# Kernel tuning notes

Hardware: AMD Instinct MI355X
Metric: run time of the kernel (lower is better)

Reference implementation:

```python
import jax, jax.numpy as jnp
import numpy as np

D_MODEL = 256
D_STATE = 64
D_CONV = 4
EXPAND = 2
HEADDIM = 64
D_INNER = EXPAND * D_MODEL          # 512
NHEADS = D_INNER // HEADDIM         # 8
CONV_CH = D_INNER + 2 * D_STATE     # 640 (x, B, C channels go through depthwise conv)
D_IN_PROJ = 2 * D_INNER + 2 * D_STATE + NHEADS  # 1160


def _dwconv_causal(x, w, b):
    # x: (b, L, ch); w: (ch, 1, k) depthwise; left-pad k-1 -> causal, same as torch pad+truncate
    out = jax.lax.conv_general_dilated(
        x.transpose(0, 2, 1), w, (1,), [(D_CONV - 1, 0)],
        dimension_numbers=('NCH', 'OIH', 'NCH'), feature_group_count=CONV_CH)
    return out.transpose(0, 2, 1) + b


def _mamba2(u, in_w, conv_w, conv_b, dt_bias, A_log, D, norm_w, out_w):
    # u: (b, L, d_model). Faithful Mamba2 block (ngroups=1, rmsnorm gated, no proj biases).
    b, L, _ = u.shape
    zxbcdt = u @ in_w.T                                   # (b, L, 1160)
    z = zxbcdt[..., :D_INNER]
    xBC = zxbcdt[..., D_INNER:D_INNER + CONV_CH]
    dt = zxbcdt[..., D_INNER + CONV_CH:]                  # (b, L, h)
    xBC = jax.nn.silu(_dwconv_causal(xBC, conv_w, conv_b))
    x = xBC[..., :D_INNER].reshape(b, L, NHEADS, HEADDIM)  # (b, L, h, p)
    Bm = xBC[..., D_INNER:D_INNER + D_STATE]              # (b, L, n)
    Cm = xBC[..., D_INNER + D_STATE:]                     # (b, L, n)
    dt = jax.nn.softplus(dt + dt_bias)                    # (b, L, h)
    dA = jnp.exp(dt * (-jnp.exp(A_log)))                  # (b, L, h)

    def step(h, inp):
        dA_t, x_t, B_t, dt_t, C_t = inp
        # h: (b, heads, p, n) selective-scan state
        h = h * dA_t[:, :, None, None] + (dt_t[:, :, None] * x_t)[..., None] * B_t[:, None, None, :]
        return h, jnp.einsum('bhpn,bn->bhp', h, C_t)

    h0 = jnp.zeros((b, NHEADS, HEADDIM, D_STATE), u.dtype)
    xs = (dA.transpose(1, 0, 2), x.transpose(1, 0, 2, 3), Bm.transpose(1, 0, 2),
          dt.transpose(1, 0, 2), Cm.transpose(1, 0, 2))
    _, ys = jax.lax.scan(step, h0, xs)                    # (L, b, h, p)
    y = ys.transpose(1, 0, 2, 3) + x * D[None, None, :, None]
    y = y.reshape(b, L, D_INNER) * jax.nn.silu(z)         # gated
    y = y * jax.lax.rsqrt(jnp.mean(y * y, axis=-1, keepdims=True) + 1e-5) * norm_w
    return y @ out_w.T                                    # (b, L, d_model)


def setup_inputs() -> dict:
    key = jax.random.key(0)
    ks = jax.random.split(key, 20)
    def mk(i, shape, s=0.02):
        return jax.random.normal(ks[i], shape, jnp.float32) * s
    inp = {"x": jax.random.normal(ks[0], (8, 64, 64, D_MODEL), jnp.float32)}
    for pre, off in (("mh", 1), ("mv", 9)):
        inp[pre + "_in_w"] = mk(off, (D_IN_PROJ, D_MODEL))
        inp[pre + "_conv_w"] = mk(off + 1, (CONV_CH, 1, D_CONV), 0.2)
        inp[pre + "_conv_b"] = jnp.zeros((CONV_CH,), jnp.float32)
        inp[pre + "_dt_bias"] = mk(off + 3, (NHEADS,), 0.5)
        inp[pre + "_A_log"] = jnp.log(jax.random.uniform(ks[off + 4], (NHEADS,), jnp.float32, 1.0, 16.0))
        inp[pre + "_D"] = jnp.ones((NHEADS,), jnp.float32)
        inp[pre + "_norm_w"] = jnp.ones((D_INNER,), jnp.float32)
        inp[pre + "_out_w"] = mk(off + 7, (D_MODEL, D_INNER))
    inp["fc_w"] = mk(17, (D_MODEL, 4 * D_MODEL))
    inp["fc_b"] = jnp.zeros((D_MODEL,), jnp.float32)
    return inp


def reference(x, mh_in_w, mh_conv_w, mh_conv_b, mh_dt_bias, mh_A_log, mh_D, mh_norm_w, mh_out_w,
              mv_in_w, mv_conv_w, mv_conv_b, mv_dt_bias, mv_A_log, mv_D, mv_norm_w, mv_out_w,
              fc_w, fc_b):
    B, H, W, C = x.shape
    mh = (mh_in_w, mh_conv_w, mh_conv_b, mh_dt_bias, mh_A_log, mh_D, mh_norm_w, mh_out_w)
    mv = (mv_in_w, mv_conv_w, mv_conv_b, mv_dt_bias, mv_A_log, mv_D, mv_norm_w, mv_out_w)
    # horizontal: rows as sequences
    x_h = x.reshape(B * H, W, C)
    h1 = _mamba2(x_h, *mh)
    # NOTE: source flips dims=[0] (merged batch*row axis), replicated faithfully
    h2 = jnp.flip(_mamba2(jnp.flip(x_h, axis=0), *mh), axis=0)
    h = jnp.concatenate([h1, h2], axis=-1).reshape(B, H, W, -1)
    # vertical: columns as sequences
    x_v = x.transpose(0, 2, 1, 3).reshape(B * W, H, C)
    v1 = _mamba2(x_v, *mv)
    v2 = jnp.flip(_mamba2(jnp.flip(x_v, axis=0), *mv), axis=0)
    v = jnp.concatenate([v1, v2], axis=-1).reshape(B, W, H, -1).transpose(0, 2, 1, 3)
    out = jnp.concatenate([v, h], axis=-1)                # (B, H, W, 4*d_model)
    return out @ fc_w.T + fc_b                            # (B, H, W, d_model)
```

## Files before the change

kernel.cpp:

```cpp
#include <hip/hip_runtime.h>
#include <hip/hip_bf16.h>


#define NTH 512

typedef __attribute__((ext_vector_type(8))) short short8;
typedef __attribute__((ext_vector_type(4))) short short4v;
typedef __attribute__((ext_vector_type(4))) float floatx4;

__device__ __forceinline__ short f2bs(float v){
  __hip_bfloat16 h = __float2bfloat16(v);
  return *reinterpret_cast<short*>(&h);
}
__device__ __forceinline__ unsigned int pk2(float lo, float hi){
  return (unsigned int)(unsigned short)f2bs(lo)
       | ((unsigned int)(unsigned short)f2bs(hi) << 16);
}
__device__ __forceinline__ float bs2f(short s){
  union { unsigned int u; float f; } c; c.u = ((unsigned int)(unsigned short)s) << 16; return c.f;
}
__device__ __forceinline__ float bhi(unsigned int u){
  union { unsigned int u; float f; } c; c.u = u & 0xffff0000u; return c.f;
}
__device__ __forceinline__ float blo(unsigned int u){
  union { unsigned int u; float f; } c; c.u = u << 16; return c.f;
}
__device__ __forceinline__ float silu_f(float v){
  return v * __builtin_amdgcn_rcpf(1.f + __expf(-v));
}
__device__ __forceinline__ float softplus_f(float v){
  return fmaxf(v, 0.f) + log1pf(__expf(-fabsf(v)));
}

__global__ void setup_weights(const float* __restrict__ fc_w,
                              const float* __restrict__ how, const float* __restrict__ hnw,
                              const float* __restrict__ vow, const float* __restrict__ vnw,
                              const float* __restrict__ hw, const float* __restrict__ vw,
                              __hip_bfloat16* __restrict__ Wc,
                              __hip_bfloat16* __restrict__ inw)
{
  int b = blockIdx.x;
  if (b < 512) {
    __shared__ float fs[2][256];
    int dir = b >> 8;
    int rr = b & 255;
    int o0 = (rr >> 1) * 2;
    int j = (rr & 1) * 256 + threadIdx.x;
    const float* ow = dir ? vow : how;
    const float* nw = dir ? vnw : hnw;
    int off = dir ? 0 : 512;
    const float* fr0 = fc_w + o0 * 1024 + off;
    const float* fr1 = fc_w + (o0 + 1) * 1024 + off;
    fs[0][threadIdx.x] = fr0[threadIdx.x] + fr0[256 + threadIdx.x];
    fs[1][threadIdx.x] = fr1[threadIdx.x] + fr1[256 + threadIdx.x];
    __syncthreads();
    float a00 = 0.f, a01 = 0.f, a02 = 0.f, a03 = 0.f;
    float a10 = 0.f, a11 = 0.f, a12 = 0.f, a13 = 0.f;
#pragma unroll 4
    for (int k = 0; k < 256; k += 4) {
      float w0 = ow[(k + 0) * 512 + j];
      float w1 = ow[(k + 1) * 512 + j];
      float w2 = ow[(k + 2) * 512 + j];
      float w3 = ow[(k + 3) * 512 + j];
      a00 += fs[0][k + 0] * w0; a01 += fs[0][k + 1] * w1;
      a02 += fs[0][k + 2] * w2; a03 += fs[0][k + 3] * w3;
      a10 += fs[1][k + 0] * w0; a11 += fs[1][k + 1] * w1;
      a12 += fs[1][k + 2] * w2; a13 += fs[1][k + 3] * w3;
    }
    float nwj = nw[j];
    Wc[(dir * 256 + o0) * 512 + j]     = __float2bfloat16(nwj * (a00 + a01 + a02 + a03));
    Wc[(dir * 256 + o0 + 1) * 512 + j] = __float2bfloat16(nwj * (a10 + a11 + a12 + a13));
  } else {
    int id = (b - 512) * 256 + threadIdx.x;
    int dir = id / 299008;
    int r = id % 299008;
    int row = r >> 8;
    const float* src = dir ? vw : hw;
    float v = (row < 1160) ? src[r] : 0.f;
    inw[id] = __float2bfloat16(v);
  }
}

#define OFS_U    0
#define OFS_R1   16896
#define OFS_BX0  25872
#define OFS_BX1  30480
#define OFS_CUM  35088
#define OFS_DT   36112
#define SM_SHORTS 36624

template<int DIR>
__global__ __launch_bounds__(NTH, 4)
void mamba_dir_kernel(const float* __restrict__ x,
                      const __hip_bfloat16* __restrict__ inw_bf,
                      const float* __restrict__ conv_w,
                      const float* __restrict__ conv_b,
                      const float* __restrict__ dt_bias,
                      const float* __restrict__ A_log,
                      const float* __restrict__ Dvec,
                      const __hip_bfloat16* __restrict__ Wc,
                      const float* __restrict__ fc_b,
                      float* __restrict__ out)
{
  __shared__ short sm[SM_SHORTS];
  short* smU  = sm + OFS_U;
  short* smR1 = sm + OFS_R1;
  short* smB  = sm + OFS_BX0;
  short* smM  = smB;
  short* smg  = smB;
  short* smC  = sm + OFS_BX1;
  short* smX  = smC;
  float* smCUM = (float*)(sm + OFS_CUM);
  short* smDT  = sm + OFS_DT;
  float* smF   = (float*)sm;

  const int tid = threadIdx.x;
  const int t = tid & 63;
  const int w = tid >> 6;
  const int lane15 = tid & 15;
  const int quad = (tid & 63) >> 4;
  const int s = blockIdx.x;

  auto MF = [](short8 a, short8 b, floatx4 c) -> floatx4 {
    return __builtin_amdgcn_mfma_f32_16x16x32_bf16(a, b, c, 0, 0, 0);
  };
  auto ldA_u = [&](int mt_, int kt) -> short8 {
    return *(const short8*)(smU + (mt_ * 16 + lane15) * 264 + kt * 32 + quad * 8);
  };
  auto ldB_w = [&](int row0, int kt) -> short8 {
    return *(const short8*)((const short*)inw_bf + (row0 + lane15) * 256 + kt * 32 + quad * 8);
  };
  auto ldB_wc = [&](int o0, int hd, int kt) -> short8 {
    return *(const short8*)((const short*)Wc + (o0 + lane15) * 512 + hd * 64 + kt * 32 + quad * 8);
  };
  auto ld72 = [&](const short* base, int row, int kt) -> short8 {
    return *(const short8*)(base + row * 72 + kt * 32 + quad * 8);
  };
  auto proj_tile = [&](int row0, short* dst, bool wr) {
    floatx4 a0 = (floatx4)0.f, a1 = (floatx4)0.f, a2 = (floatx4)0.f, a3 = (floatx4)0.f;
#pragma unroll
    for (int kt = 0; kt < 8; ++kt) {
      short8 b = ldB_w(row0, kt);
      a0 = MF(ldA_u(0, kt), b, a0);
      a1 = MF(ldA_u(1, kt), b, a1);
      a2 = MF(ldA_u(2, kt), b, a2);
      a3 = MF(ldA_u(3, kt), b, a3);
    }
    if (wr) {
      *(unsigned int*)(dst + 0)  = pk2(a0[0], a0[1]);
      *(unsigned int*)(dst + 2)  = pk2(a0[2], a0[3]);
      *(unsigned int*)(dst + 16) = pk2(a1[0], a1[1]);
      *(unsigned int*)(dst + 18) = pk2(a1[2], a1[3]);
      *(unsigned int*)(dst + 32) = pk2(a2[0], a2[1]);
      *(unsigned int*)(dst + 34) = pk2(a2[2], a2[3]);
      *(unsigned int*)(dst + 48) = pk2(a3[0], a3[1]);
      *(unsigned int*)(dst + 50) = pk2(a3[2], a3[3]);
    }
  };

  long ubase; int ustride;
  if (DIR == 0) { ubase = (long)s * 16384; ustride = 256; }
  else { ubase = (long)(s >> 6) * 1048576 + (long)(s & 63) * 256; ustride = 16384; }

  for (int i = tid; i < 4096; i += NTH) {
    int tt = i >> 6, c4 = (i & 63) * 4;
    const float4 xa = *(const float4*)(x + ubase + (long)tt * ustride + c4);
    uint2 pk; pk.x = pk2(xa.x, xa.y); pk.y = pk2(xa.z, xa.w);
    *(uint2*)((unsigned int*)smU + tt * 132 + (i & 63) * 2) = pk;
  }
  if (tid < 64) smF[tid * 132 + 128] = 0.f;
  __syncthreads();

  for (int jt = w; jt < 9; jt += 8) {
    int q = jt * 16 + lane15;
    proj_tile(1024 + jt * 16, smR1 + q * 66 + quad * 4, q < 136);
  }
  __syncthreads();

  {
    int q = tid & 127;
    int tg = tid >> 7;
    const float4 cw = *(const float4*)(conv_w + (512 + q) * 4);
    float cb = conv_b[512 + q];
    const short* rowp = smR1 + q * 66;
    short* dstB = (q < 64) ? (smB + q) : (smC + (q - 64));
#pragma unroll
    for (int k = 0; k < 4; ++k) {
      int t0 = tg * 4 + k;
      const short* bp = rowp + 4 * t0 - 4;
      unsigned int u0 = *(const unsigned int*)(bp + 0);
      unsigned int u1 = *(const unsigned int*)(bp + 2);
      unsigned int u2 = *(const unsigned int*)(bp + 4);
      unsigned int u3 = *(const unsigned int*)(bp + 6);
      float f1 = bhi(u0), f2 = blo(u1), f3 = bhi(u1), f4 = blo(u2);
      float f5 = bhi(u2), f6 = blo(u3), f7 = bhi(u3);
      if (t0 == 0) { f1 = 0.f; f2 = 0.f; f3 = 0.f; }
      float v0 = fmaf(cw.x, f1, fmaf(cw.y, f2, fmaf(cw.z, f3, fmaf(cw.w, f4, cb))));
      float v1 = fmaf(cw.x, f2, fmaf(cw.y, f3, fmaf(cw.z, f4, fmaf(cw.w, f5, cb))));
      float v2 = fmaf(cw.x, f3, fmaf(cw.y, f4, fmaf(cw.z, f5, fmaf(cw.w, f6, cb))));
      float v3 = fmaf(cw.x, f4, fmaf(cw.y, f5, fmaf(cw.z, f6, fmaf(cw.w, f7, cb))));
      int tt = 4 * t0;
      dstB[(tt + 0) * 72] = f2bs(silu_f(v0));
      dstB[(tt + 1) * 72] = f2bs(silu_f(v1));
      dstB[(tt + 2) * 72] = f2bs(silu_f(v2));
      dstB[(tt + 3) * 72] = f2bs(silu_f(v3));
    }
    float dtv = softplus_f(bs2f(smR1[(128 + w) * 66 + t]) + dt_bias[w]);
    smDT[w * 64 + t] = f2bs(dtv);
    float cum = -__expf(A_log[w]) * dtv;
#pragma unroll
    for (int off = 1; off < 64; off <<= 1) {
      float y = __shfl_up(cum, off, 64);
      if (t >= off) cum += y;
    }
    smCUM[w * 64 + t] = cum;
  }
  __syncthreads();

  const int mt = w >> 1, nt0 = (w & 1) * 2;
  floatx4 g0 = (floatx4)0.f, g1 = (floatx4)0.f;
#pragma unroll
  for (int kt = 0; kt < 2; ++kt) {
    short8 a  = ld72(smC, mt * 16 + lane15, kt);
    short8 b0 = ld72(smB, nt0 * 16 + lane15, kt);
    short8 b1 = ld72(smB, (nt0 + 1) * 16 + lane15, kt);
    g0 = MF(a, b0, g0); g1 = MF(a, b1, g1);
  }

  float ssqAcc = 0.f;
  floatx4 accO[4][2];
#pragma unroll
  for (int m = 0; m < 4; ++m) { accO[m][0] = (floatx4)0.f; accO[m][1] = (floatx4)0.f; }

  for (int hd = 0; hd < 8; ++hd) {
    {
      int row0 = (w < 4) ? (hd * 64 + w * 16) : (512 + hd * 64 + (w - 4) * 16);
      int q = ((w < 4) ? w * 16 : 64 + (w - 4) * 16) + lane15;
      proj_tile(row0, smR1 + q * 66 + quad * 4, true);
    }
    __syncthreads();

    {
      int p = t;
      int ch = hd * 64 + p;
      const float4 cw = *(const float4*)(conv_w + ch * 4);
      float cb = conv_b[ch];
      const short* rowp = smR1 + (64 + p) * 66;
      short* dstX = smX + p * 72;
#pragma unroll
      for (int k = 0; k < 2; ++k) {
        int t0 = w * 2 + k;
        const short* bp = rowp + 4 * t0 - 4;
        unsigned int u0 = *(const unsigned int*)(bp + 0);
        unsigned int u1 = *(const unsigned int*)(bp + 2);
        unsigned int u2 = *(const unsigned int*)(bp + 4);
        unsigned int u3 = *(const unsigned int*)(bp + 6);
        float f1 = bhi(u0), f2 = blo(u1), f3 = bhi(u1), f4 = blo(u2);
        float f5 = bhi(u2), f6 = blo(u3), f7 = bhi(u3);
        if (t0 == 0) { f1 = 0.f; f2 = 0.f; f3 = 0.f; }
        float v0 = fmaf(cw.x, f1, fmaf(cw.y, f2, fmaf(cw.z, f3, fmaf(cw.w, f4, cb))));
        float v1 = fmaf(cw.x, f2, fmaf(cw.y, f3, fmaf(cw.z, f4, fmaf(cw.w, f5, cb))));
        float v2 = fmaf(cw.x, f3, fmaf(cw.y, f4, fmaf(cw.z, f5, fmaf(cw.w, f6, cb))));
        float v3 = fmaf(cw.x, f4, fmaf(cw.y, f5, fmaf(cw.z, f6, fmaf(cw.w, f7, cb))));
        *(unsigned int*)(dstX + 4 * t0)     = pk2(silu_f(v0), silu_f(v1));
        *(unsigned int*)(dstX + 4 * t0 + 2) = pk2(silu_f(v2), silu_f(v3));
      }
      const float* cumh = smCUM + hd * 64;
      const short* dth  = smDT + hd * 64;
#pragma unroll
      for (int j = 0; j < 2; ++j) {
        floatx4 gv = j ? g1 : g0;
        int ss = (nt0 + j) * 16 + lane15;
        float cums = cumh[ss];
        float dts  = bs2f(dth[ss]);
#pragma unroll
        for (int r = 0; r < 4; ++r) {
          int tt = mt * 16 + quad * 4 + r;
          float m = (tt >= ss) ? __expf(cumh[tt] - cums) * dts * gv[r] : 0.f;
          smM[tt * 72 + ss] = f2bs(m);
        }
      }
    }
    __syncthreads();

    floatx4 y0 = (floatx4)0.f, y1 = (floatx4)0.f;
#pragma unroll
    for (int kt = 0; kt < 2; ++kt) {
      short8 a  = ld72(smM, mt * 16 + lane15, kt);
      short8 b0 = ld72(smX, nt0 * 16 + lane15, kt);
      short8 b1 = ld72(smX, (nt0 + 1) * 16 + lane15, kt);
      y0 = MF(a, b0, y0); y1 = MF(a, b1, y1);
    }
    __syncthreads();

    {
      float Dh = Dvec[hd];
#pragma unroll
      for (int j = 0; j < 2; ++j) {
        floatx4 yy = j ? y1 : y0;
        int p = (nt0 + j) * 16 + lane15;
        short4v xv4 = *(const short4v*)(smX + p * 72 + mt * 16 + quad * 4);
#pragma unroll
        for (int r = 0; r < 4; ++r) {
          int tr = mt * 16 + quad * 4 + r;
          float xv = bs2f(xv4[r]);
          float zv = bs2f(smR1[p * 66 + tr]);
          float g = (yy[r] + Dh * xv) * silu_f(zv);
          smg[tr * 72 + p] = f2bs(g);
        }
      }
    }
    __syncthreads();

    {
      short8 gv = *(const short8*)(smg + t * 72 + w * 8);
#pragma unroll
      for (int j = 0; j < 8; ++j) { float g = bs2f(gv[j]); ssqAcc += g * g; }
    }
#pragma unroll
    for (int kt = 0; kt < 2; ++kt) {
      short8 b0 = ldB_wc(w * 16, hd, kt);
      short8 b1 = ldB_wc((w + 8) * 16, hd, kt);
#pragma unroll
      for (int m = 0; m < 4; ++m) {
        short8 a = ld72(smg, m * 16 + lane15, kt);
        accO[m][0] = MF(a, b0, accO[m][0]);
        accO[m][1] = MF(a, b1, accO[m][1]);
      }
    }
  }

  atomicAdd(&smF[t * 132 + 128], ssqAcc);
  __syncthreads();
  if (tid < 64)
    smF[tid * 132 + 129] = rsqrtf(smF[tid * 132 + 128] * (1.f / 512.f) + 1e-5f);
  __syncthreads();

#pragma unroll
  for (int m = 0; m < 4; ++m) {
#pragma unroll
    for (int n = 0; n < 2; ++n) {
      int o = (w + n * 8) * 16 + lane15;
#pragma unroll
      for (int r = 0; r < 4; ++r) {
        int tt = m * 16 + quad * 4 + r;
        float val = accO[m][n][r] * smF[tt * 132 + 129];
        long rowg = (DIR == 0) ? ((long)s * 64 + tt)
                               : ((long)(s >> 6) * 4096 + (long)tt * 64 + (s & 63));
        long gi = rowg * 256 + o;
        if (DIR == 0) out[gi] = fc_b[o] + val;
        else          out[gi] += val;
      }
    }
  }
}

extern "C" void kernel_launch(void* const* d_in, const int* in_sizes, int n_in,
                              void* d_out, int out_size, void* d_ws, size_t ws_size,
                              hipStream_t stream) {
  const float* x          = (const float*)d_in[0];
  const float* mh_in_w    = (const float*)d_in[1];
  const float* mh_conv_w  = (const float*)d_in[2];
  const float* mh_conv_b  = (const float*)d_in[3];
  const float* mh_dt_bias = (const float*)d_in[4];
  const float* mh_A_log   = (const float*)d_in[5];
  const float* mh_D       = (const float*)d_in[6];
  const float* mh_norm_w  = (const float*)d_in[7];
  const float* mh_out_w   = (const float*)d_in[8];
  const float* mv_in_w    = (const float*)d_in[9];
  const float* mv_conv_w  = (const float*)d_in[10];
  const float* mv_conv_b  = (const float*)d_in[11];
  const float* mv_dt_bias = (const float*)d_in[12];
  const float* mv_A_log   = (const float*)d_in[13];
  const float* mv_D       = (const float*)d_in[14];
  const float* mv_norm_w  = (const float*)d_in[15];
  const float* mv_out_w   = (const float*)d_in[16];
  const float* fc_w       = (const float*)d_in[17];
  const float* fc_b       = (const float*)d_in[18];
  float* out = (float*)d_out;

  __hip_bfloat16* Wcb  = (__hip_bfloat16*)d_ws;
  __hip_bfloat16* inwb = (__hip_bfloat16*)((char*)d_ws + 524288);

  setup_weights<<<2848, 256, 0, stream>>>(fc_w, mh_out_w, mh_norm_w, mv_out_w, mv_norm_w,
                                          mh_in_w, mv_in_w, Wcb, inwb);
  mamba_dir_kernel<0><<<512, NTH, 0, stream>>>(x, inwb, mh_conv_w, mh_conv_b,
      mh_dt_bias, mh_A_log, mh_D, Wcb, fc_b, out);
  mamba_dir_kernel<1><<<512, NTH, 0, stream>>>(x, inwb + 299008, mv_conv_w, mv_conv_b,
      mv_dt_bias, mv_A_log, mv_D, Wcb + 131072, fc_b, out);
}
```

Before: 291.0 us.

## Fuse both scan directions into one launch with atomic output and 32x32 MFMA projections

Merges the horizontal and vertical Mamba kernels into a single 1024-block launch so both directions run concurrently instead of serially. The output is now pre-filled with fc_b in the setup kernel and both directions accumulate into it with float atomics. The in-projection tiles switch from 16x16x32 to 32x32x16 MFMA, which means fewer instructions and more reuse of the B operand. The cost is atomic traffic on the output and nondeterministic summation order.

```diff
diff --git a/kernel.cpp b/kernel.cpp
--- a/kernel.cpp
+++ b/kernel.cpp
@@ -7,6 +7,7 @@
 typedef __attribute__((ext_vector_type(8))) short short8;
 typedef __attribute__((ext_vector_type(4))) short short4v;
 typedef __attribute__((ext_vector_type(4))) float floatx4;
+typedef __attribute__((ext_vector_type(16))) float floatx16;
 
 __device__ __forceinline__ short f2bs(float v){
   __hip_bfloat16 h = __float2bfloat16(v);
@@ -36,8 +37,10 @@
                               const float* __restrict__ how, const float* __restrict__ hnw,
                               const float* __restrict__ vow, const float* __restrict__ vnw,
                               const float* __restrict__ hw, const float* __restrict__ vw,
+                              const float* __restrict__ fc_b,
                               __hip_bfloat16* __restrict__ Wc,
-                              __hip_bfloat16* __restrict__ inw)
+                              __hip_bfloat16* __restrict__ inw,
+                              float* __restrict__ out)
 {
   int b = blockIdx.x;
   if (b < 512) {
@@ -70,7 +73,7 @@
     float nwj = nw[j];
     Wc[(dir * 256 + o0) * 512 + j]     = __float2bfloat16(nwj * (a00 + a01 + a02 + a03));
     Wc[(dir * 256 + o0 + 1) * 512 + j] = __float2bfloat16(nwj * (a10 + a11 + a12 + a13));
-  } else {
+  } else if (b < 2848) {
     int id = (b - 512) * 256 + threadIdx.x;
     int dir = id / 299008;
     int r = id % 299008;
@@ -78,6 +81,10 @@
     const float* src = dir ? vw : hw;
     float v = (row < 1160) ? src[r] : 0.f;
     inw[id] = __float2bfloat16(v);
+  } else {
+    int id = (b - 2848) * 256 + threadIdx.x;
+    int i4 = id * 4;
+    *(float4*)(out + i4) = *(const float4*)(fc_b + (i4 & 255));
   }
 }
 
@@ -89,18 +96,16 @@
 #define OFS_DT   36112
 #define SM_SHORTS 36624
 
-template<int DIR>
 __global__ __launch_bounds__(NTH, 4)
-void mamba_dir_kernel(const float* __restrict__ x,
-                      const __hip_bfloat16* __restrict__ inw_bf,
-                      const float* __restrict__ conv_w,
-                      const float* __restrict__ conv_b,
-                      const float* __restrict__ dt_bias,
-                      const float* __restrict__ A_log,
-                      const float* __restrict__ Dvec,
-                      const __hip_bfloat16* __restrict__ Wc,
-                      const float* __restrict__ fc_b,
-                      float* __restrict__ out)
+void mamba_fused(const float* __restrict__ x,
+                 const __hip_bfloat16* __restrict__ inw_all,
+                 const float* __restrict__ hconv_w, const float* __restrict__ vconv_w,
+                 const float* __restrict__ hconv_b, const float* __restrict__ vconv_b,
+                 const float* __restrict__ hdt_b,  const float* __restrict__ vdt_b,
+                 const float* __restrict__ hA,     const float* __restrict__ vA,
+                 const float* __restrict__ hD,     const float* __restrict__ vD,
+                 const __hip_bfloat16* __restrict__ Wc_all,
+                 float* __restrict__ out)
 {
   __shared__ short sm[SM_SHORTS];
   short* smU  = sm + OFS_U;
@@ -119,16 +124,29 @@
   const int w = tid >> 6;
   const int lane15 = tid & 15;
   const int quad = (tid & 63) >> 4;
-  const int s = blockIdx.x;
+
+  const int DIR = blockIdx.x >> 9;
+  const int s = blockIdx.x & 511;
+
+  const __hip_bfloat16* inw = inw_all + DIR * 299008;
+  const __hip_bfloat16* Wc  = Wc_all  + DIR * 131072;
+  const float* conv_w  = DIR ? vconv_w : hconv_w;
+  const float* conv_b  = DIR ? vconv_b : hconv_b;
+  const float* dt_bias = DIR ? vdt_b  : hdt_b;
+  const float* A_log   = DIR ? vA     : hA;
+  const float* Dvec    = DIR ? vD     : hD;
 
   auto MF = [](short8 a, short8 b, floatx4 c) -> floatx4 {
     return __builtin_amdgcn_mfma_f32_16x16x32_bf16(a, b, c, 0, 0, 0);
   };
+  auto MF32 = [](short8 a, short8 b, floatx16 c) -> floatx16 {
+    return __builtin_amdgcn_mfma_f32_32x32x16_bf16(a, b, c, 0, 0, 0);
+  };
   auto ldA_u = [&](int mt_, int kt) -> short8 {
     return *(const short8*)(smU + (mt_ * 16 + lane15) * 264 + kt * 32 + quad * 8);
   };
   auto ldB_w = [&](int row0, int kt) -> short8 {
-    return *(const short8*)((const short*)inw_bf + (row0 + lane15) * 256 + kt * 32 + quad * 8);
+    return *(const short8*)((const short*)inw + (row0 + lane15) * 256 + kt * 32 + quad * 8);
   };
   auto ldB_wc = [&](int o0, int hd, int kt) -> short8 {
     return *(const short8*)((const short*)Wc + (o0 + lane15) * 512 + hd * 64 + kt * 32 + quad * 8);
@@ -158,6 +176,31 @@
     }
   };
 
+  const int ct  = w & 3;
+  const int mt2 = w >> 2;
+  const int lane31 = tid & 31;
+  const int half32 = (tid & 63) >> 5;
+  const short* A32 = smU + (mt2 * 32 + lane31) * 264 + half32 * 8;
+  auto proj32 = [&](int wrow0, int c0) {
+    const short* Bb = (const short*)inw + (wrow0 + lane31) * 256 + half32 * 8;
+    floatx16 aA = (floatx16)0.f, aB = (floatx16)0.f;
+#pragma unroll
+    for (int kt = 0; kt < 16; kt += 2) {
+      aA = MF32(*(const short8*)(A32 + kt * 16),      *(const short8*)(Bb + kt * 16),      aA);
+      aB = MF32(*(const short8*)(A32 + kt * 16 + 16), *(const short8*)(Bb + kt * 16 + 16), aB);
+    }
+    short* dst = smR1 + (c0 + lane31) * 66 + mt2 * 32 + 4 * half32;
+#pragma unroll
+    for (int g = 0; g < 4; ++g) {
+      float e0 = aA[4*g+0] + aB[4*g+0];
+      float e1 = aA[4*g+1] + aB[4*g+1];
+      float e2 = aA[4*g+2] + aB[4*g+2];
+      float e3 = aA[4*g+3] + aB[4*g+3];
+      *(unsigned int*)(dst + g * 8)     = pk2(e0, e1);
+      *(unsigned int*)(dst + g * 8 + 2) = pk2(e2, e3);
+    }
+  };
+
   long ubase; int ustride;
   if (DIR == 0) { ubase = (long)s * 16384; ustride = 256; }
   else { ubase = (long)(s >> 6) * 1048576 + (long)(s & 63) * 256; ustride = 16384; }
@@ -171,10 +214,9 @@
   if (tid < 64) smF[tid * 132 + 128] = 0.f;
   __syncthreads();
 
-  for (int jt = w; jt < 9; jt += 8) {
-    int q = jt * 16 + lane15;
-    proj_tile(1024 + jt * 16, smR1 + q * 66 + quad * 4, q < 136);
-  }
+  proj32(1024 + ct * 32, ct * 32);
+  if (w == 7)
+    proj_tile(1152, smR1 + (128 + lane15) * 66 + quad * 4, lane15 < 8);
   __syncthreads();
 
   {
@@ -234,9 +276,9 @@
 
   for (int hd = 0; hd < 8; ++hd) {
     {
-      int row0 = (w < 4) ? (hd * 64 + w * 16) : (512 + hd * 64 + (w - 4) * 16);
-      int q = ((w < 4) ? w * 16 : 64 + (w - 4) * 16) + lane15;
-      proj_tile(row0, smR1 + q * 66 + quad * 4, true);
+      int c0 = ct * 32;
+      int wrow0 = (c0 < 64) ? (hd * 64 + c0) : (512 + hd * 64 + (c0 - 64));
+      proj32(wrow0, c0);
     }
     __syncthreads();
 
@@ -347,9 +389,7 @@
         float val = accO[m][n][r] * smF[tt * 132 + 129];
         long rowg = (DIR == 0) ? ((long)s * 64 + tt)
                                : ((long)(s >> 6) * 4096 + (long)tt * 64 + (s & 63));
-        long gi = rowg * 256 + o;
-        if (DIR == 0) out[gi] = fc_b[o] + val;
-        else          out[gi] += val;
+        atomicAdd(&out[rowg * 256 + o], val);
       }
     }
   }
@@ -382,10 +422,10 @@
   __hip_bfloat16* Wcb  = (__hip_bfloat16*)d_ws;
   __hip_bfloat16* inwb = (__hip_bfloat16*)((char*)d_ws + 524288);
 
-  setup_weights<<<2848, 256, 0, stream>>>(fc_w, mh_out_w, mh_norm_w, mv_out_w, mv_norm_w,
-                                          mh_in_w, mv_in_w, Wcb, inwb);
-  mamba_dir_kernel<0><<<512, NTH, 0, stream>>>(x, inwb, mh_conv_w, mh_conv_b,
-      mh_dt_bias, mh_A_log, mh_D, Wcb, fc_b, out);
-  mamba_dir_kernel<1><<<512, NTH, 0, stream>>>(x, inwb + 299008, mv_conv_w, mv_conv_b,
-      mv_dt_bias, mv_A_log, mv_D, Wcb + 131072, fc_b, out);
-}
+  setup_weights<<<11040, 256, 0, stream>>>(fc_w, mh_out_w, mh_norm_w, mv_out_w, mv_norm_w,
+                                           mh_in_w, mv_in_w, fc_b, Wcb, inwb, out);
+  mamba_fused<<<1024, NTH, 0, stream>>>(x, inwb,
+      mh_conv_w, mv_conv_w, mh_conv_b, mv_conv_b,
+      mh_dt_bias, mv_dt_bias, mh_A_log, mv_A_log, mh_D, mv_D,
+      Wcb, out);
+}
```

Result: slower. 357.7 us (+22.9%).

## XOR-swizzle shared-memory tiles to avoid bank conflicts; vectorize weight conversion

Applied to the files above, without the earlier changes.

Applies an XOR swizzle to the LDS layouts of the input tile, the B/C/X buffers, the decay matrix and the gated output. Every writer and reader, including the MFMA operand loads, is updated to match. The goal is fewer bank conflicts on the 16-byte MFMA fragment loads and on the strided scalar stores. The weight-conversion part of setup_weights now handles 8 elements per thread with float4 loads and short8 stores, which shrinks that launch's grid. The risk is a correctness bug if any access to a swizzled buffer was missed, because all of them must agree.

```diff
diff --git a/kernel.cpp b/kernel.cpp
--- a/kernel.cpp
+++ b/kernel.cpp
@@ -71,13 +71,21 @@
     Wc[(dir * 256 + o0) * 512 + j]     = __float2bfloat16(nwj * (a00 + a01 + a02 + a03));
     Wc[(dir * 256 + o0 + 1) * 512 + j] = __float2bfloat16(nwj * (a10 + a11 + a12 + a13));
   } else {
-    int id = (b - 512) * 256 + threadIdx.x;
-    int dir = id / 299008;
-    int r = id % 299008;
+    int id8 = ((b - 512) * 256 + threadIdx.x) * 8;
+    int dir = id8 / 299008;
+    int r = id8 % 299008;
     int row = r >> 8;
     const float* src = dir ? vw : hw;
-    float v = (row < 1160) ? src[r] : 0.f;
-    inw[id] = __float2bfloat16(v);
+    short8 o;
+    if (row < 1160) {
+      const float4 x0 = *(const float4*)(src + r);
+      const float4 x1 = *(const float4*)(src + r + 4);
+      o[0] = f2bs(x0.x); o[1] = f2bs(x0.y); o[2] = f2bs(x0.z); o[3] = f2bs(x0.w);
+      o[4] = f2bs(x1.x); o[5] = f2bs(x1.y); o[6] = f2bs(x1.z); o[7] = f2bs(x1.w);
+    } else {
+      o = (short8)0;
+    }
+    *(short8*)((short*)inw + id8) = o;
   }
 }
 
@@ -125,7 +133,8 @@
     return __builtin_amdgcn_mfma_f32_16x16x32_bf16(a, b, c, 0, 0, 0);
   };
   auto ldA_u = [&](int mt_, int kt) -> short8 {
-    return *(const short8*)(smU + (mt_ * 16 + lane15) * 264 + kt * 32 + quad * 8);
+    return *(const short8*)(smU + (mt_ * 16 + lane15) * 264 + kt * 32
+                            + ((quad ^ (lane15 & 3)) << 3));
   };
   auto ldB_w = [&](int row0, int kt) -> short8 {
     return *(const short8*)((const short*)inw_bf + (row0 + lane15) * 256 + kt * 32 + quad * 8);
@@ -134,7 +143,7 @@
     return *(const short8*)((const short*)Wc + (o0 + lane15) * 512 + hd * 64 + kt * 32 + quad * 8);
   };
   auto ld72 = [&](const short* base, int row, int kt) -> short8 {
-    return *(const short8*)(base + row * 72 + kt * 32 + quad * 8);
+    return *(const short8*)(base + row * 72 + kt * 32 + ((quad ^ (row & 3)) << 3));
   };
   auto proj_tile = [&](int row0, short* dst, bool wr) {
     floatx4 a0 = (floatx4)0.f, a1 = (floatx4)0.f, a2 = (floatx4)0.f, a3 = (floatx4)0.f;
@@ -166,7 +175,8 @@
     int tt = i >> 6, c4 = (i & 63) * 4;
     const float4 xa = *(const float4*)(x + ubase + (long)tt * ustride + c4);
     uint2 pk; pk.x = pk2(xa.x, xa.y); pk.y = pk2(xa.z, xa.w);
-    *(uint2*)((unsigned int*)smU + tt * 132 + (i & 63) * 2) = pk;
+    int dw = (2 * (i & 63)) ^ ((tt & 3) << 2);
+    *(uint2*)((unsigned int*)smU + tt * 132 + dw) = pk;
   }
   if (tid < 64) smF[tid * 132 + 128] = 0.f;
   __syncthreads();
@@ -183,7 +193,8 @@
     const float4 cw = *(const float4*)(conv_w + (512 + q) * 4);
     float cb = conv_b[512 + q];
     const short* rowp = smR1 + q * 66;
-    short* dstB = (q < 64) ? (smB + q) : (smC + (q - 64));
+    short* dstB; int qc;
+    if (q < 64) { dstB = smB; qc = q; } else { dstB = smC; qc = q - 64; }
 #pragma unroll
     for (int k = 0; k < 4; ++k) {
       int t0 = tg * 4 + k;
@@ -200,10 +211,10 @@
       float v2 = fmaf(cw.x, f3, fmaf(cw.y, f4, fmaf(cw.z, f5, fmaf(cw.w, f6, cb))));
       float v3 = fmaf(cw.x, f4, fmaf(cw.y, f5, fmaf(cw.z, f6, fmaf(cw.w, f7, cb))));
       int tt = 4 * t0;
-      dstB[(tt + 0) * 72] = f2bs(silu_f(v0));
-      dstB[(tt + 1) * 72] = f2bs(silu_f(v1));
-      dstB[(tt + 2) * 72] = f2bs(silu_f(v2));
-      dstB[(tt + 3) * 72] = f2bs(silu_f(v3));
+      dstB[(tt + 0) * 72 + qc]        = f2bs(silu_f(v0));
+      dstB[(tt + 1) * 72 + (qc ^ 8)]  = f2bs(silu_f(v1));
+      dstB[(tt + 2) * 72 + (qc ^ 16)] = f2bs(silu_f(v2));
+      dstB[(tt + 3) * 72 + (qc ^ 24)] = f2bs(silu_f(v3));
     }
     float dtv = softplus_f(bs2f(smR1[(128 + w) * 66 + t]) + dt_bias[w]);
     smDT[w * 64 + t] = f2bs(dtv);
@@ -247,6 +258,7 @@
       float cb = conv_b[ch];
       const short* rowp = smR1 + (64 + p) * 66;
       short* dstX = smX + p * 72;
+      const int xsw = (p & 3) << 3;
 #pragma unroll
       for (int k = 0; k < 2; ++k) {
         int t0 = w * 2 + k;
@@ -262,8 +274,9 @@
         float v1 = fmaf(cw.x, f2, fmaf(cw.y, f3, fmaf(cw.z, f4, fmaf(cw.w, f5, cb))));
         float v2 = fmaf(cw.x, f3, fmaf(cw.y, f4, fmaf(cw.z, f5, fmaf(cw.w, f6, cb))));
         float v3 = fmaf(cw.x, f4, fmaf(cw.y, f5, fmaf(cw.z, f6, fmaf(cw.w, f7, cb))));
-        *(unsigned int*)(dstX + 4 * t0)     = pk2(silu_f(v0), silu_f(v1));
-        *(unsigned int*)(dstX + 4 * t0 + 2) = pk2(silu_f(v2), silu_f(v3));
+        int xc = (4 * t0) ^ xsw;
+        *(unsigned int*)(dstX + xc)     = pk2(silu_f(v0), silu_f(v1));
+        *(unsigned int*)(dstX + xc + 2) = pk2(silu_f(v2), silu_f(v3));
       }
       const float* cumh = smCUM + hd * 64;
       const short* dth  = smDT + hd * 64;
@@ -277,7 +290,7 @@
         for (int r = 0; r < 4; ++r) {
           int tt = mt * 16 + quad * 4 + r;
           float m = (tt >= ss) ? __expf(cumh[tt] - cums) * dts * gv[r] : 0.f;
-          smM[tt * 72 + ss] = f2bs(m);
+          smM[tt * 72 + (ss ^ (r << 3))] = f2bs(m);
         }
       }
     }
@@ -299,21 +312,22 @@
       for (int j = 0; j < 2; ++j) {
         floatx4 yy = j ? y1 : y0;
         int p = (nt0 + j) * 16 + lane15;
-        short4v xv4 = *(const short4v*)(smX + p * 72 + mt * 16 + quad * 4);
+        short4v xv4 = *(const short4v*)(smX + p * 72
+                        + ((mt * 16 + quad * 4) ^ ((p & 3) << 3)));
 #pragma unroll
         for (int r = 0; r < 4; ++r) {
           int tr = mt * 16 + quad * 4 + r;
           float xv = bs2f(xv4[r]);
           float zv = bs2f(smR1[p * 66 + tr]);
           float g = (yy[r] + Dh * xv) * silu_f(zv);
-          smg[tr * 72 + p] = f2bs(g);
+          smg[tr * 72 + (p ^ (r << 3))] = f2bs(g);
         }
       }
     }
     __syncthreads();
 
     {
-      short8 gv = *(const short8*)(smg + t * 72 + w * 8);
+      short8 gv = *(const short8*)(smg + t * 72 + ((w ^ (t & 3)) << 3));
 #pragma unroll
       for (int j = 0; j < 8; ++j) { float g = bs2f(gv[j]); ssqAcc += g * g; }
     }
@@ -382,8 +396,8 @@
   __hip_bfloat16* Wcb  = (__hip_bfloat16*)d_ws;
   __hip_bfloat16* inwb = (__hip_bfloat16*)((char*)d_ws + 524288);
 
-  setup_weights<<<2848, 256, 0, stream>>>(fc_w, mh_out_w, mh_norm_w, mv_out_w, mv_norm_w,
-                                          mh_in_w, mv_in_w, Wcb, inwb);
+  setup_weights<<<804, 256, 0, stream>>>(fc_w, mh_out_w, mh_norm_w, mv_out_w, mv_norm_w,
+                                         mh_in_w, mv_in_w, Wcb, inwb);
   mamba_dir_kernel<0><<<512, NTH, 0, stream>>>(x, inwb, mh_conv_w, mh_conv_b,
       mh_dt_bias, mh_A_log, mh_D, Wcb, fc_b, out);
   mamba_dir_kernel<1><<<512, NTH, 0, stream>>>(x, inwb + 299008, mv_conv_w, mv_conv_b,
```

Result: slower. 298.8 us (+2.7%).

## Keep A-operand fragments in registers and vectorize weight conversion

Applied to the files above, without the earlier changes.

The in-projection GEMM is restructured so that each wave owns one 16-row M tile of the input. The wave loads its eight A fragments from LDS into registers once and reuses them across all output column tiles, where previously every wave reread all four M tiles from LDS for each column tile. The bf16 conversion in weight setup is also vectorized to process 8 elements per thread, cutting its grid from 2848 to 804 blocks. The trade-off is higher register pressure from holding the A fragments, and each B weight fragment is now loaded from global memory by four waves instead of one.

```diff
diff --git a/kernel.cpp b/kernel.cpp
--- a/kernel.cpp
+++ b/kernel.cpp
@@ -71,13 +71,21 @@
     Wc[(dir * 256 + o0) * 512 + j]     = __float2bfloat16(nwj * (a00 + a01 + a02 + a03));
     Wc[(dir * 256 + o0 + 1) * 512 + j] = __float2bfloat16(nwj * (a10 + a11 + a12 + a13));
   } else {
-    int id = (b - 512) * 256 + threadIdx.x;
-    int dir = id / 299008;
-    int r = id % 299008;
+    int id8 = ((b - 512) * 256 + threadIdx.x) * 8;
+    int dir = id8 / 299008;
+    int r = id8 % 299008;
     int row = r >> 8;
     const float* src = dir ? vw : hw;
-    float v = (row < 1160) ? src[r] : 0.f;
-    inw[id] = __float2bfloat16(v);
+    short8 o;
+    if (row < 1160) {
+      const float4 x0 = *(const float4*)(src + r);
+      const float4 x1 = *(const float4*)(src + r + 4);
+      o[0] = f2bs(x0.x); o[1] = f2bs(x0.y); o[2] = f2bs(x0.z); o[3] = f2bs(x0.w);
+      o[4] = f2bs(x1.x); o[5] = f2bs(x1.y); o[6] = f2bs(x1.z); o[7] = f2bs(x1.w);
+    } else {
+      o = (short8)0;
+    }
+    *(short8*)((short*)inw + id8) = o;
   }
 }
 
@@ -124,9 +132,6 @@
   auto MF = [](short8 a, short8 b, floatx4 c) -> floatx4 {
     return __builtin_amdgcn_mfma_f32_16x16x32_bf16(a, b, c, 0, 0, 0);
   };
-  auto ldA_u = [&](int mt_, int kt) -> short8 {
-    return *(const short8*)(smU + (mt_ * 16 + lane15) * 264 + kt * 32 + quad * 8);
-  };
   auto ldB_w = [&](int row0, int kt) -> short8 {
     return *(const short8*)((const short*)inw_bf + (row0 + lane15) * 256 + kt * 32 + quad * 8);
   };
@@ -136,27 +141,6 @@
   auto ld72 = [&](const short* base, int row, int kt) -> short8 {
     return *(const short8*)(base + row * 72 + kt * 32 + quad * 8);
   };
-  auto proj_tile = [&](int row0, short* dst, bool wr) {
-    floatx4 a0 = (floatx4)0.f, a1 = (floatx4)0.f, a2 = (floatx4)0.f, a3 = (floatx4)0.f;
-#pragma unroll
-    for (int kt = 0; kt < 8; ++kt) {
-      short8 b = ldB_w(row0, kt);
-      a0 = MF(ldA_u(0, kt), b, a0);
-      a1 = MF(ldA_u(1, kt), b, a1);
-      a2 = MF(ldA_u(2, kt), b, a2);
-      a3 = MF(ldA_u(3, kt), b, a3);
-    }
-    if (wr) {
-      *(unsigned int*)(dst + 0)  = pk2(a0[0], a0[1]);
-      *(unsigned int*)(dst + 2)  = pk2(a0[2], a0[3]);
-      *(unsigned int*)(dst + 16) = pk2(a1[0], a1[1]);
-      *(unsigned int*)(dst + 18) = pk2(a1[2], a1[3]);
-      *(unsigned int*)(dst + 32) = pk2(a2[0], a2[1]);
-      *(unsigned int*)(dst + 34) = pk2(a2[2], a2[3]);
-      *(unsigned int*)(dst + 48) = pk2(a3[0], a3[1]);
-      *(unsigned int*)(dst + 50) = pk2(a3[2], a3[3]);
-    }
-  };
 
   long ubase; int ustride;
   if (DIR == 0) { ubase = (long)s * 16384; ustride = 256; }
@@ -171,9 +155,26 @@
   if (tid < 64) smF[tid * 132 + 128] = 0.f;
   __syncthreads();
 
-  for (int jt = w; jt < 9; jt += 8) {
-    int q = jt * 16 + lane15;
-    proj_tile(1024 + jt * 16, smR1 + q * 66 + quad * 4, q < 136);
+  const int amt = w & 3;
+  const int g   = w >> 2;
+  short8 av[8];
+#pragma unroll
+  for (int kt = 0; kt < 8; ++kt)
+    av[kt] = *(const short8*)(smU + (amt * 16 + lane15) * 264 + kt * 32 + quad * 8);
+
+  auto storeC = [&](floatx4 a, int q) {
+    short* dst = smR1 + q * 66 + amt * 16 + quad * 4;
+    *(unsigned int*)(dst + 0) = pk2(a[0], a[1]);
+    *(unsigned int*)(dst + 2) = pk2(a[2], a[3]);
+  };
+
+  for (int c = g; c < 9; c += 2) {
+    floatx4 acc = (floatx4)0.f;
+#pragma unroll
+    for (int kt = 0; kt < 8; ++kt)
+      acc = MF(av[kt], ldB_w(1024 + c * 16, kt), acc);
+    int q = c * 16 + lane15;
+    if (q < 136) storeC(acc, q);
   }
   __syncthreads();
 
@@ -234,9 +235,22 @@
 
   for (int hd = 0; hd < 8; ++hd) {
     {
-      int row0 = (w < 4) ? (hd * 64 + w * 16) : (512 + hd * 64 + (w - 4) * 16);
-      int q = ((w < 4) ? w * 16 : 64 + (w - 4) * 16) + lane15;
-      proj_tile(row0, smR1 + q * 66 + quad * 4, true);
+      int wb = g ? (512 + hd * 64) : (hd * 64);
+      int qb = g * 64;
+#pragma unroll
+      for (int jp = 0; jp < 2; ++jp) {
+        int r0 = wb + (jp * 2) * 16, r1 = wb + (jp * 2 + 1) * 16;
+        floatx4 A0 = (floatx4)0.f, A1 = (floatx4)0.f;
+#pragma unroll
+        for (int kt = 0; kt < 8; ++kt) {
+          short8 b0 = ldB_w(r0, kt);
+          short8 b1 = ldB_w(r1, kt);
+          A0 = MF(av[kt], b0, A0);
+          A1 = MF(av[kt], b1, A1);
+        }
+        storeC(A0, qb + (jp * 2) * 16 + lane15);
+        storeC(A1, qb + (jp * 2 + 1) * 16 + lane15);
+      }
     }
     __syncthreads();
 
@@ -382,8 +396,8 @@
   __hip_bfloat16* Wcb  = (__hip_bfloat16*)d_ws;
   __hip_bfloat16* inwb = (__hip_bfloat16*)((char*)d_ws + 524288);
 
-  setup_weights<<<2848, 256, 0, stream>>>(fc_w, mh_out_w, mh_norm_w, mv_out_w, mv_norm_w,
-                                          mh_in_w, mv_in_w, Wcb, inwb);
+  setup_weights<<<804, 256, 0, stream>>>(fc_w, mh_out_w, mh_norm_w, mv_out_w, mv_norm_w,
+                                         mh_in_w, mv_in_w, Wcb, inwb);
   mamba_dir_kernel<0><<<512, NTH, 0, stream>>>(x, inwb, mh_conv_w, mh_conv_b,
       mh_dt_bias, mh_A_log, mh_D, Wcb, fc_b, out);
   mamba_dir_kernel<1><<<512, NTH, 0, stream>>>(x, inwb + 299008, mv_conv_w, mv_conv_b,
```

After: 449.7 us. 54.5% more time.
